# Kernel tuning notes

Hardware: AMD Instinct MI355X
Metric: run time of the kernel (lower is better)

Reference implementation:

```python
import jax, jax.numpy as jnp
import numpy as np

N = 100000   # num nodes
E = 800000   # num edges (random-walk metapath graph)
IN = 256     # in_size
H = 8        # layer_num_heads
D = 32       # out_size per head
HD = H * D   # 256, semantic attention in_size
HID = 128    # semantic attention hidden
NEG_SLOPE = 0.2  # DGL GATConv leaky_relu slope


def setup_inputs() -> dict:
    key = jax.random.key(0)
    ks = jax.random.split(key, 10)
    h = jax.random.normal(ks[0], (N, IN), dtype=jnp.float32)
    src = jax.random.randint(ks[1], (E,), 0, N)
    dst = jax.random.randint(ks[2], (E,), 0, N)
    s = 0.05
    W_fc = jax.random.normal(ks[3], (IN, HD), dtype=jnp.float32) * s
    attn_l = jax.random.normal(ks[4], (H, D), dtype=jnp.float32) * s
    attn_r = jax.random.normal(ks[5], (H, D), dtype=jnp.float32) * s
    bias = jnp.zeros((HD,), dtype=jnp.float32)
    sem_W1 = jax.random.normal(ks[6], (HD, HID), dtype=jnp.float32) * s
    sem_b1 = jnp.zeros((HID,), dtype=jnp.float32)
    sem_W2 = jax.random.normal(ks[7], (HID, 1), dtype=jnp.float32) * s
    return {"h": h, "W_fc": W_fc, "attn_l": attn_l, "attn_r": attn_r,
            "bias": bias, "sem_W1": sem_W1, "sem_b1": sem_b1,
            "sem_W2": sem_W2, "src": src, "dst": dst}


def _gat(h, W_fc, attn_l, attn_r, bias, src, dst):
    feat = (h @ W_fc).reshape(N, H, D)                      # [N,H,D]
    el = jnp.sum(feat * attn_l, axis=-1)                    # [N,H]
    er = jnp.sum(feat * attn_r, axis=-1)                    # [N,H]
    e = jax.nn.leaky_relu(el[src] + er[dst], NEG_SLOPE)     # [E,H]
    # edge softmax over incoming edges per destination node
    mx = jax.ops.segment_max(e, dst, num_segments=N)        # [N,H], -inf for isolated
    mx = jnp.where(jnp.isfinite(mx), mx, 0.0)
    ee = jnp.exp(e - mx[dst])                               # [E,H]
    denom = jax.ops.segment_sum(ee, dst, num_segments=N)    # [N,H]
    alpha = ee / denom[dst]                                 # [E,H]
    msg = feat[src] * alpha[:, :, None]                     # [E,H,D] gather+weight
    rst = jax.ops.segment_sum(msg, dst, num_segments=N)     # [N,H,D] scatter-add
    rst = rst + bias.reshape(H, D)
    return jax.nn.elu(rst).reshape(N, HD)                   # activation=F.elu, flatten(1)


def reference(h, W_fc, attn_l, attn_r, bias, sem_W1, sem_b1, sem_W2, src, dst):
    out = _gat(h, W_fc, attn_l, attn_r, bias, src, dst)     # [N, HD]
    z = out[:, None, :]                                     # [N, 1, HD] single metapath
    w = (jnp.tanh(z @ sem_W1 + sem_b1) @ sem_W2).mean(0)    # [1, 1]
    beta = jax.nn.softmax(w, axis=0)                        # [1, 1]
    return jnp.sum(beta * z, axis=1)                        # [N, HD]
```

## Files before the change

kernel.cpp:

```cpp
#include <hip/hip_runtime.h>
#include <math.h>


#define NN 100000
#define NE 800000

typedef __attribute__((ext_vector_type(8))) short bf16x8;
typedef __attribute__((ext_vector_type(4))) float f32x4;

__device__ __forceinline__ unsigned short f2b(float f){
  unsigned u = __float_as_uint(f);
  return (unsigned short)((u + 0x7FFFu + ((u >> 16) & 1u)) >> 16);
}
__device__ __forceinline__ float b2f(unsigned short b){
  return __uint_as_float(((unsigned)b) << 16);
}

__global__ void k_prep(const float* __restrict__ W, unsigned short* __restrict__ Wt,
                       int* __restrict__ cnt, int* __restrict__ cur){
  int i = blockIdx.x * 256 + threadIdx.x;
  if (i < 65536){ int n = i >> 8, k = i & 255; Wt[n * 256 + k] = f2b(W[k * 256 + n]); }
  if (i < NN){ cnt[i] = 0; cur[i] = 0; }
}

__global__ __launch_bounds__(256) void k_gemm(const float* __restrict__ A,
    const unsigned short* __restrict__ Wt, unsigned short* __restrict__ feat){
  __shared__ unsigned short lA[64][40];
  __shared__ unsigned short lB[256][40];
  const int t = threadIdx.x;
  const int lane = t & 63;
  const int wave = t >> 6;
  const int wm = wave >> 1, wn = wave & 1;
  const int bm = blockIdx.x * 64;
  const int l15 = lane & 15, lg = lane >> 4;

  f32x4 acc[2][8];
  #pragma unroll
  for (int i = 0; i < 2; ++i)
    #pragma unroll
    for (int j = 0; j < 8; ++j){ f32x4 z = {0.f,0.f,0.f,0.f}; acc[i][j] = z; }

  const int arow = t >> 2, ac8 = (t & 3) * 8;
  const int gr = bm + arow;

  float4 a0, a1; uint4 bw[4];
#define LOADG(KT) do {                                                        \
    float4 z4 = {0.f,0.f,0.f,0.f}; a0 = z4; a1 = z4;                          \
    if (gr < NN){                                                             \
      const float* p = A + (size_t)gr * 256 + (KT) * 32 + ac8;                \
      a0 = *(const float4*)p; a1 = *(const float4*)(p + 4);                   \
    }                                                                         \
    _Pragma("unroll")                                                         \
    for (int i_ = 0; i_ < 4; ++i_){                                           \
      int c = i_ * 256 + t;                                                   \
      bw[i_] = *(const uint4*)(Wt + (size_t)(c >> 2) * 256 + (KT) * 32 + (c & 3) * 8); \
    }                                                                         \
  } while (0)

  LOADG(0);
  for (int kt = 0; kt < 8; ++kt){
    __syncthreads();
    {
      uint4 av;
      av.x = (unsigned)f2b(a0.x) | ((unsigned)f2b(a0.y) << 16);
      av.y = (unsigned)f2b(a0.z) | ((unsigned)f2b(a0.w) << 16);
      av.z = (unsigned)f2b(a1.x) | ((unsigned)f2b(a1.y) << 16);
      av.w = (unsigned)f2b(a1.z) | ((unsigned)f2b(a1.w) << 16);
      *(uint4*)&lA[arow][ac8] = av;
      #pragma unroll
      for (int i = 0; i < 4; ++i){
        int c = i * 256 + t;
        *(uint4*)&lB[c >> 2][(c & 3) * 8] = bw[i];
      }
    }
    __syncthreads();
    if (kt < 7) LOADG(kt + 1);
    bf16x8 af0 = *(const bf16x8*)&lA[wm * 32 + l15][lg * 8];
    bf16x8 af1 = *(const bf16x8*)&lA[wm * 32 + 16 + l15][lg * 8];
    #pragma unroll
    for (int ni = 0; ni < 8; ++ni){
      bf16x8 bf = *(const bf16x8*)&lB[wn * 128 + ni * 16 + l15][lg * 8];
      acc[0][ni] = __builtin_amdgcn_mfma_f32_16x16x32_bf16(af0, bf, acc[0][ni], 0, 0, 0);
      acc[1][ni] = __builtin_amdgcn_mfma_f32_16x16x32_bf16(af1, bf, acc[1][ni], 0, 0, 0);
    }
  }
#undef LOADG
  #pragma unroll
  for (int mi = 0; mi < 2; ++mi){
    #pragma unroll
    for (int ni = 0; ni < 8; ++ni){
      int c = wn * 128 + ni * 16 + l15;
      int r0 = bm + wm * 32 + mi * 16 + lg * 4;
      #pragma unroll
      for (int reg = 0; reg < 4; ++reg){
        int r = r0 + reg;
        if (r < NN) feat[(size_t)r * 256 + c] = f2b(acc[mi][ni][reg]);
      }
    }
  }
}

__global__ void k_elr(const unsigned short* __restrict__ feat,
                      const float* __restrict__ attn_l, const float* __restrict__ attn_r,
                      float* __restrict__ el, float* __restrict__ er){
  int i = blockIdx.x * 256 + threadIdx.x;
  if (i >= NN * 8) return;
  int h = i & 7;
  const unsigned short* f = feat + (size_t)i * 32;
  const float* al = attn_l + h * 32;
  const float* ar = attn_r + h * 32;
  float sl = 0.f, sr = 0.f;
  #pragma unroll
  for (int j = 0; j < 4; ++j){
    uint4 v = *(const uint4*)(f + j * 8);
    unsigned vv[4] = {v.x, v.y, v.z, v.w};
    #pragma unroll
    for (int q = 0; q < 4; ++q){
      float x0 = b2f((unsigned short)(vv[q] & 0xffffu));
      float x1 = b2f((unsigned short)(vv[q] >> 16));
      int d = j * 8 + q * 2;
      sl += x0 * al[d] + x1 * al[d + 1];
      sr += x0 * ar[d] + x1 * ar[d + 1];
    }
  }
  el[i] = sl; er[i] = sr;
}

__global__ void k_edge1(const int* __restrict__ dst, int* __restrict__ cnt){
  int e = blockIdx.x * 256 + threadIdx.x;
  if (e < NE) atomicAdd(&cnt[dst[e]], 1);
}

__global__ __launch_bounds__(1024) void k_scanA(const int* __restrict__ cnt,
    int* __restrict__ partial, int* __restrict__ bsum){
  __shared__ int lds[1024];
  int t = threadIdx.x;
  int i = blockIdx.x * 1024 + t;
  int v = (i < NN) ? cnt[i] : 0;
  lds[t] = v;
  __syncthreads();
  for (int off = 1; off < 1024; off <<= 1){
    int add = (t >= off) ? lds[t - off] : 0;
    __syncthreads();
    lds[t] += add;
    __syncthreads();
  }
  if (i < NN) partial[i] = lds[t] - v;
  if (t == 1023) bsum[blockIdx.x] = lds[1023];
}

__global__ __launch_bounds__(128) void k_scanB(const int* __restrict__ bsum,
                                               int* __restrict__ boff, int nb){
  __shared__ int lds[128];
  int t = threadIdx.x;
  int v = (t < nb) ? bsum[t] : 0;
  lds[t] = v;
  __syncthreads();
  for (int off = 1; off < 128; off <<= 1){
    int add = (t >= off) ? lds[t - off] : 0;
    __syncthreads();
    lds[t] += add;
    __syncthreads();
  }
  if (t < nb) boff[t] = lds[t] - v;
}

__global__ void k_edge2(const int* __restrict__ src, const int* __restrict__ dst,
                        const int* __restrict__ partial, const int* __restrict__ boff,
                        int* __restrict__ cur, int* __restrict__ csr_src){
  int e = blockIdx.x * 256 + threadIdx.x;
  if (e >= NE) return;
  int s = src[e], d = dst[e];
  int slot = partial[d] + boff[d >> 10] + atomicAdd(&cur[d], 1);
  csr_src[slot] = s;
}

__device__ __forceinline__ void acc8(float* a, uint4 f, float w){
  unsigned u[4] = {f.x, f.y, f.z, f.w};
  #pragma unroll
  for (int j = 0; j < 4; ++j){
    a[2 * j]     += w * __uint_as_float(u[j] << 16);
    a[2 * j + 1] += w * __uint_as_float(u[j] & 0xffff0000u);
  }
}

__global__ __launch_bounds__(256) void k_agg(const int* __restrict__ csr_src,
    const float* __restrict__ el, const float* __restrict__ er,
    const unsigned short* __restrict__ feat, const int* __restrict__ partial,
    const int* __restrict__ boff, const float* __restrict__ bias, float* __restrict__ out){
  int n = blockIdx.x * 4 + (threadIdx.x >> 6);
  if (n >= NN) return;
  const int t = threadIdx.x & 63;
  const int half = t >> 5;
  const int q = t & 31;
  const int h = q >> 2;
  int beg = partial[n] + boff[n >> 10];
  int end = (n + 1 < NN) ? (partial[n + 1] + boff[(n + 1) >> 10]) : NE;
  float ern = er[(size_t)n * 8 + h];
  float den = 0.f;
  float a[8] = {0.f,0.f,0.f,0.f,0.f,0.f,0.f,0.f};
  const unsigned short* fb = feat + q * 8;

  int i = beg;
  for (; i + 4 <= end; i += 4){
    int s0 = csr_src[i + half];
    int s1 = csr_src[i + 2 + half];
    uint4 f0 = *(const uint4*)(fb + (size_t)s0 * 256);
    uint4 f1 = *(const uint4*)(fb + (size_t)s1 * 256);
    float e0 = el[(size_t)s0 * 8 + h] + ern;
    float e1 = el[(size_t)s1 * 8 + h] + ern;
    e0 = e0 > 0.f ? e0 : 0.2f * e0;  e0 = __expf(e0);
    e1 = e1 > 0.f ? e1 : 0.2f * e1;  e1 = __expf(e1);
    den += e0 + e1;
    acc8(a, f0, e0);
    acc8(a, f1, e1);
  }
  for (; i < end; i += 2){
    int ia = i + half;
    if (ia < end){
      int s = csr_src[ia];
      uint4 f = *(const uint4*)(fb + (size_t)s * 256);
      float e = el[(size_t)s * 8 + h] + ern;
      e = e > 0.f ? e : 0.2f * e;  e = __expf(e);
      den += e;
      acc8(a, f, e);
    }
  }
  den += __shfl_xor(den, 32);
  #pragma unroll
  for (int j = 0; j < 8; ++j) a[j] += __shfl_xor(a[j], 32);
  float inv = den > 0.f ? 1.f / den : 0.f;

  const float* bp = bias + q * 8 + half * 4;
  float4 o;
  #pragma unroll
  for (int j = 0; j < 4; ++j){
    float v = (half ? a[4 + j] : a[j]) * inv + bp[j];
    ((float*)&o)[j] = v > 0.f ? v : expm1f(v);
  }
  *(float4*)(out + (size_t)n * 256 + q * 8 + half * 4) = o;
}

extern "C" void kernel_launch(void* const* d_in, const int* in_sizes, int n_in,
                              void* d_out, int out_size, void* d_ws, size_t ws_size,
                              hipStream_t stream){
  (void)in_sizes; (void)n_in; (void)out_size; (void)ws_size;
  const float* h      = (const float*)d_in[0];
  const float* W_fc   = (const float*)d_in[1];
  const float* attn_l = (const float*)d_in[2];
  const float* attn_r = (const float*)d_in[3];
  const float* bias   = (const float*)d_in[4];
  const int* src = (const int*)d_in[8];
  const int* dst = (const int*)d_in[9];
  float* out = (float*)d_out;

  char* w = (char*)d_ws;
  auto alloc = [&](size_t b){ char* p = w; w += (b + 255) & ~(size_t)255; return p; };
  unsigned short* feat = (unsigned short*)alloc((size_t)NN * 256 * 2);
  unsigned short* Wt   = (unsigned short*)alloc(256 * 256 * 2);
  float* el      = (float*)alloc((size_t)NN * 8 * 4);
  float* er      = (float*)alloc((size_t)NN * 8 * 4);
  int*   cnt     = (int*)alloc((size_t)NN * 4);
  int*   cur     = (int*)alloc((size_t)NN * 4);
  int*   partial = (int*)alloc((size_t)NN * 4);
  int*   bsum    = (int*)alloc(128 * 4);
  int*   boff    = (int*)alloc(128 * 4);
  int*   csr_src = (int*)alloc((size_t)NE * 4);

  const int nb = (NN + 1023) / 1024;

  k_prep <<<(NN + 255) / 256, 256, 0, stream>>>(W_fc, Wt, cnt, cur);
  k_gemm <<<(NN + 63) / 64, 256, 0, stream>>>(h, Wt, feat);
  k_elr  <<<(NN * 8 + 255) / 256, 256, 0, stream>>>(feat, attn_l, attn_r, el, er);
  k_edge1<<<(NE + 255) / 256, 256, 0, stream>>>(dst, cnt);
  k_scanA<<<nb, 1024, 0, stream>>>(cnt, partial, bsum);
  k_scanB<<<1, 128, 0, stream>>>(bsum, boff, nb);
  k_edge2<<<(NE + 255) / 256, 256, 0, stream>>>(src, dst, partial, boff, cur, csr_src);
  k_agg  <<<(NN + 3) / 4, 256, 0, stream>>>(csr_src, el, er, feat, partial, boff, bias, out);
}
```

Baseline: 466.0 us.

## Restructure GEMM to keep A fragments in registers and stage swizzled W halves

The GEMM kernel now loads each wave's 32 rows of A straight from global memory into registers as bf16 fragments covering the whole K dimension, so the A tile no longer goes through shared memory. W is staged into 64KB of LDS in two 128-column halves with an XOR swizzle to avoid bank conflicts. Each block covers 128 rows instead of 64, which reduces how often W is reloaded. The trade-offs are higher register pressure (64 VGPRs for A fragments plus the accumulators) and large LDS use, which may lower occupancy, and the K-loop no longer has the previous load/compute double-buffering.

```diff
diff --git a/kernel.cpp b/kernel.cpp
--- a/kernel.cpp
+++ b/kernel.cpp
@@ -25,76 +25,73 @@
 
 __global__ __launch_bounds__(256) void k_gemm(const float* __restrict__ A,
     const unsigned short* __restrict__ Wt, unsigned short* __restrict__ feat){
-  __shared__ unsigned short lA[64][40];
-  __shared__ unsigned short lB[256][40];
+  __shared__ unsigned short lB[32768];
   const int t = threadIdx.x;
   const int lane = t & 63;
   const int wave = t >> 6;
-  const int wm = wave >> 1, wn = wave & 1;
-  const int bm = blockIdx.x * 64;
   const int l15 = lane & 15, lg = lane >> 4;
-
-  f32x4 acc[2][8];
-  #pragma unroll
-  for (int i = 0; i < 2; ++i)
-    #pragma unroll
-    for (int j = 0; j < 8; ++j){ f32x4 z = {0.f,0.f,0.f,0.f}; acc[i][j] = z; }
-
-  const int arow = t >> 2, ac8 = (t & 3) * 8;
-  const int gr = bm + arow;
-
-  float4 a0, a1; uint4 bw[4];
-#define LOADG(KT) do {                                                        \
-    float4 z4 = {0.f,0.f,0.f,0.f}; a0 = z4; a1 = z4;                          \
-    if (gr < NN){                                                             \
-      const float* p = A + (size_t)gr * 256 + (KT) * 32 + ac8;                \
-      a0 = *(const float4*)p; a1 = *(const float4*)(p + 4);                   \
-    }                                                                         \
-    _Pragma("unroll")                                                         \
-    for (int i_ = 0; i_ < 4; ++i_){                                           \
-      int c = i_ * 256 + t;                                                   \
-      bw[i_] = *(const uint4*)(Wt + (size_t)(c >> 2) * 256 + (KT) * 32 + (c & 3) * 8); \
-    }                                                                         \
-  } while (0)
-
-  LOADG(0);
+  const int bm = blockIdx.x * 128;
+  const int m0 = bm + wave * 32;
+
+  bf16x8 afr[8][2];
+  #pragma unroll
   for (int kt = 0; kt < 8; ++kt){
-    __syncthreads();
-    {
-      uint4 av;
-      av.x = (unsigned)f2b(a0.x) | ((unsigned)f2b(a0.y) << 16);
-      av.y = (unsigned)f2b(a0.z) | ((unsigned)f2b(a0.w) << 16);
-      av.z = (unsigned)f2b(a1.x) | ((unsigned)f2b(a1.y) << 16);
-      av.w = (unsigned)f2b(a1.z) | ((unsigned)f2b(a1.w) << 16);
-      *(uint4*)&lA[arow][ac8] = av;
+    #pragma unroll
+    for (int mi = 0; mi < 2; ++mi){
+      int r = m0 + mi * 16 + l15;
+      float4 x = {0.f,0.f,0.f,0.f}, y = x;
+      if (r < NN){
+        const float* p = A + (size_t)r * 256 + kt * 32 + lg * 8;
+        x = *(const float4*)p; y = *(const float4*)(p + 4);
+      }
+      union { bf16x8 v; unsigned u[4]; } pk;
+      pk.u[0] = (unsigned)f2b(x.x) | ((unsigned)f2b(x.y) << 16);
+      pk.u[1] = (unsigned)f2b(x.z) | ((unsigned)f2b(x.w) << 16);
+      pk.u[2] = (unsigned)f2b(y.x) | ((unsigned)f2b(y.y) << 16);
+      pk.u[3] = (unsigned)f2b(y.z) | ((unsigned)f2b(y.w) << 16);
+      afr[kt][mi] = pk.v;
+    }
+  }
+
+  for (int c = 0; c < 2; ++c){
+    if (c) __syncthreads();
+    #pragma unroll
+    for (int i = 0; i < 16; ++i){
+      int flat = i * 256 + t;
+      int n = flat >> 5, s = flat & 31;
+      uint4 v = *(const uint4*)(Wt + (((size_t)(c * 128 + n)) << 8) + s * 8);
+      *(uint4*)((char*)lB + n * 512 + ((s ^ (n & 31)) << 4)) = v;
+    }
+    __syncthreads();
+
+    f32x4 acc[2][8];
+    #pragma unroll
+    for (int i = 0; i < 2; ++i)
       #pragma unroll
-      for (int i = 0; i < 4; ++i){
-        int c = i * 256 + t;
-        *(uint4*)&lB[c >> 2][(c & 3) * 8] = bw[i];
+      for (int j = 0; j < 8; ++j){ f32x4 z = {0.f,0.f,0.f,0.f}; acc[i][j] = z; }
+
+    #pragma unroll
+    for (int kt = 0; kt < 8; ++kt){
+      #pragma unroll
+      for (int ni = 0; ni < 8; ++ni){
+        int n = ni * 16 + l15;
+        int s = kt * 4 + lg;
+        bf16x8 bfr = *(const bf16x8*)((char*)lB + n * 512 + ((s ^ (n & 31)) << 4));
+        acc[0][ni] = __builtin_amdgcn_mfma_f32_16x16x32_bf16(afr[kt][0], bfr, acc[0][ni], 0, 0, 0);
+        acc[1][ni] = __builtin_amdgcn_mfma_f32_16x16x32_bf16(afr[kt][1], bfr, acc[1][ni], 0, 0, 0);
       }
     }
-    __syncthreads();
-    if (kt < 7) LOADG(kt + 1);
-    bf16x8 af0 = *(const bf16x8*)&lA[wm * 32 + l15][lg * 8];
-    bf16x8 af1 = *(const bf16x8*)&lA[wm * 32 + 16 + l15][lg * 8];
-    #pragma unroll
-    for (int ni = 0; ni < 8; ++ni){
-      bf16x8 bf = *(const bf16x8*)&lB[wn * 128 + ni * 16 + l15][lg * 8];
-      acc[0][ni] = __builtin_amdgcn_mfma_f32_16x16x32_bf16(af0, bf, acc[0][ni], 0, 0, 0);
-      acc[1][ni] = __builtin_amdgcn_mfma_f32_16x16x32_bf16(af1, bf, acc[1][ni], 0, 0, 0);
-    }
-  }
-#undef LOADG
-  #pragma unroll
-  for (int mi = 0; mi < 2; ++mi){
-    #pragma unroll
-    for (int ni = 0; ni < 8; ++ni){
-      int c = wn * 128 + ni * 16 + l15;
-      int r0 = bm + wm * 32 + mi * 16 + lg * 4;
+    #pragma unroll
+    for (int mi = 0; mi < 2; ++mi){
       #pragma unroll
-      for (int reg = 0; reg < 4; ++reg){
-        int r = r0 + reg;
-        if (r < NN) feat[(size_t)r * 256 + c] = f2b(acc[mi][ni][reg]);
+      for (int ni = 0; ni < 8; ++ni){
+        int col = c * 128 + ni * 16 + l15;
+        int r0 = m0 + mi * 16 + lg * 4;
+        #pragma unroll
+        for (int reg = 0; reg < 4; ++reg){
+          int r = r0 + reg;
+          if (r < NN) feat[(size_t)r * 256 + col] = f2b(acc[mi][ni][reg]);
+        }
       }
     }
   }
@@ -270,7 +267,7 @@
   const int nb = (NN + 1023) / 1024;
 
   k_prep <<<(NN + 255) / 256, 256, 0, stream>>>(W_fc, Wt, cnt, cur);
-  k_gemm <<<(NN + 63) / 64, 256, 0, stream>>>(h, Wt, feat);
+  k_gemm <<<(NN + 127) / 128, 256, 0, stream>>>(h, Wt, feat);
   k_elr  <<<(NN * 8 + 255) / 256, 256, 0, stream>>>(feat, attn_l, attn_r, el, er);
   k_edge1<<<(NE + 255) / 256, 256, 0, stream>>>(dst, cnt);
   k_scanA<<<nb, 1024, 0, stream>>>(cnt, partial, bsum);
```

Measured after the change: 419.1 us. 1.11x faster.
